# Performance work log

Measured on AMD Instinct MI355X. Metric: run time of the kernel, lower is better.

The kernel has to match this reference:

```python
import jax, jax.numpy as jnp
import numpy as np

B, C, D = 512, 50000, 256
N_LOADED = 40000


def setup_inputs() -> dict:
    key = jax.random.key(0)
    k1, k2, k3, k4 = jax.random.split(key, 4)
    visual_feats = jax.random.normal(k1, (B, D), dtype=jnp.float32)
    text_feats = jax.random.normal(k2, (C, D), dtype=jnp.float32)
    # sparse multi-hot labels; force class 0 positive for every row so the
    # positive set (intersected with loaded ids) is never empty
    batch_label = (jax.random.uniform(k3, (B, C)) < 0.02).astype(jnp.int32)
    batch_label = batch_label.at[:, 0].set(1)
    # distinct loaded class ids; force id 0 to be loaded
    ids = jax.random.permutation(k4, C)[:N_LOADED].astype(jnp.int32)
    ids = jnp.sort(ids).at[0].set(0)
    return {
        "visual_feats": visual_feats,
        "text_feats": text_feats,
        "batch_label": batch_label,
        "class_ids_loaded": ids,
        "d_space": D,
    }


def reference(visual_feats, text_feats, batch_label, class_ids_loaded, d_space):
    num_classes = text_feats.shape[0]
    # membership mask for loaded class ids (the set() intersection in torch)
    loaded = jnp.zeros((num_classes,), dtype=bool).at[class_ids_loaded].set(True)

    # cosine similarity; note: torch adds 1e-6 eps only to text-feature norms
    v = visual_feats / jnp.linalg.norm(visual_feats, axis=1, keepdims=True)
    t = text_feats / (1e-6 + jnp.linalg.norm(text_feats, axis=1, keepdims=True))
    S = v @ t.T  # [B, C]

    pos = (batch_label != 0) & loaded[None, :]  # ragged positive sets, as mask
    neg = (batch_label == 0) & loaded[None, :]  # ragged negative sets, as mask

    # denominator: sum of exp(sim) over negatives, per row
    denom = jnp.sum(jnp.where(neg, jnp.exp(S), 0.0), axis=1)  # [B]
    n_pos = jnp.sum(pos, axis=1).astype(S.dtype)  # [B]

    # per-row loss: mean over positives of -log(exp(s_p)/denom) = log(denom)-s_p
    per_row = jnp.sum(jnp.where(pos, jnp.log(denom)[:, None] - S, 0.0), axis=1) / n_pos
    return jnp.mean(per_row).reshape(1)
```

## Files before the change

kernel.cpp:

```cpp
#include <hip/hip_runtime.h>
#include <math.h>

#define D_DIM 256
#define TM 128
#define TN 128
#define BK 32
#define NBP 392
#define CBPR 7
#define CBLKS (CBPR * 512)

typedef __attribute__((ext_vector_type(8))) short short8;
typedef __attribute__((ext_vector_type(4))) float floatx4;
typedef unsigned long long u64;

__device__ __forceinline__ unsigned short f2bf(float f) {
    unsigned int u = __float_as_uint(f);
    u += 0x7FFFu + ((u >> 16) & 1u);
    return (unsigned short)(u >> 16);
}

__device__ __forceinline__ void gload16(const void* g, void* lds) {
    __builtin_amdgcn_global_load_lds(
        (const __attribute__((address_space(1))) unsigned int*)g,
        (__attribute__((address_space(3))) unsigned int*)lds, 16, 0, 0);
}

__global__ __launch_bounds__(256) void prep_compress(
    const float* __restrict__ V, const float* __restrict__ T,
    const int* __restrict__ label, const int* __restrict__ ids,
    u64* __restrict__ loadedmask, u64* __restrict__ posmask,
    unsigned short* __restrict__ Vb, unsigned short* __restrict__ Tb,
    float* __restrict__ gaccum, unsigned int* __restrict__ gcount,
    int B, int C, int n_loaded, int WPR) {
    const int bid = blockIdx.x;
    const int tid = threadIdx.x;
    const int lane = tid & 63;

    if (bid < CBLKS) {
        int row = bid / CBPR;
        int sub = bid - row * CBPR;
        int wl  = tid >> 6;
        int w0col = (sub * 4 + wl) * 2048;
        if (w0col >= C) return;
        const int* lp = label + (size_t)row * C;
        int4 lo[4], hi[4];
        #pragma unroll
        for (int r = 0; r < 4; ++r) {
            int c0 = w0col + r * 512 + lane * 8;
            if (c0 < C) {
                lo[r] = *(const int4*)(lp + c0);
                hi[r] = *(const int4*)(lp + c0 + 4);
            } else {
                lo[r] = make_int4(0, 0, 0, 0);
                hi[r] = make_int4(0, 0, 0, 0);
            }
        }
        #pragma unroll
        for (int r = 0; r < 4; ++r) {
            unsigned int by =
                (lo[r].x ? 1u : 0u) | (lo[r].y ? 2u : 0u) |
                (lo[r].z ? 4u : 0u) | (lo[r].w ? 8u : 0u) |
                (hi[r].x ? 16u : 0u) | (hi[r].y ? 32u : 0u) |
                (hi[r].z ? 64u : 0u) | (hi[r].w ? 128u : 0u);
            u64 wv = (u64)by << (8 * (lane & 7));
            wv |= __shfl_xor(wv, 1);
            wv |= __shfl_xor(wv, 2);
            wv |= __shfl_xor(wv, 4);
            if ((lane & 7) == 0) {
                int wc = ((w0col + r * 512) >> 6) + (lane >> 3);
                if (wc < WPR) posmask[(size_t)row * WPR + wc] = wv;
            }
        }
        return;
    }

    int ptid = (bid - CBLKS) * 256 + tid;
    if (ptid == 0) { *gcount = 0u; *gaccum = 0.f; }
    if (ptid < WPR) {
        int base = ptid << 6;
        int lo = 0, hi = n_loaded;
        while (lo < hi) { int mid = (lo + hi) >> 1; if (ids[mid] < base) lo = mid + 1; else hi = mid; }
        u64 m = 0;
        for (int i = lo; i < n_loaded; ++i) {
            int v = ids[i]; if (v >= base + 64) break;
            m |= 1ull << (v - base);
        }
        loadedmask[ptid] = m;
    }
    int wave = ptid >> 6;
    if (wave >= B + C) return;
    bool isV = wave < B;
    const float* src = isV ? (V + (size_t)wave * D_DIM)
                           : (T + (size_t)(wave - B) * D_DIM);
    float4 x = ((const float4*)src)[lane];
    float ss = x.x * x.x + x.y * x.y + x.z * x.z + x.w * x.w;
    #pragma unroll
    for (int off = 32; off > 0; off >>= 1) ss += __shfl_xor(ss, off);
    float nrm = sqrtf(ss);
    float s = isV ? (1.0f / nrm) : (1.0f / (1e-6f + nrm));
    ushort4 o;
    o.x = f2bf(x.x * s); o.y = f2bf(x.y * s);
    o.z = f2bf(x.z * s); o.w = f2bf(x.w * s);
    unsigned short* dst = isV ? (Vb + (size_t)wave * D_DIM)
                              : (Tb + (size_t)(wave - B) * D_DIM);
    ((ushort4*)dst)[lane] = o;
}

__global__ __launch_bounds__(256) void gemm_fused(
    const unsigned short* __restrict__ Vb, const unsigned short* __restrict__ Tb,
    const u64* __restrict__ posmask, const u64* __restrict__ loadedmask,
    float* __restrict__ denomP, float* __restrict__ posP, int C, int WPR) {
    __shared__ unsigned short As[2][TM * BK];
    __shared__ unsigned short Bs[2][TN * BK];
    __shared__ float sDen[TM], sPos[TM];

    const int tid  = threadIdx.x;
    const int lane = tid & 63;
    const int w    = tid >> 6;
    const int m0 = blockIdx.x * TM;
    const int n0 = blockIdx.y * TN;

    if (tid < TM) { sDen[tid] = 0.f; sPos[tid] = 0.f; }

    const int sra = lane >> 2;
    const int kc  = (lane & 3) * 8;
    int ga  = m0 + w * 32 + sra;
    int gb0 = n0 + w * 32 + sra;
    int gb1 = gb0 + 16;
    if (gb0 >= C) gb0 = C - 1;
    if (gb1 >= C) gb1 = C - 1;
    const unsigned short* gA0 = Vb + (size_t)ga * D_DIM + kc;
    const unsigned short* gA1 = gA0 + (size_t)16 * D_DIM;
    const unsigned short* gB0 = Tb + (size_t)gb0 * D_DIM + kc;
    const unsigned short* gB1 = Tb + (size_t)gb1 * D_DIM + kc;
    const int lofsA = w * 32 * BK;
    const int lofsB = w * 32 * BK;

    const int wm = (w >> 1) * 64;
    const int wn = (w & 1) * 64;
    const int fr = lane & 15;
    const int quad = lane >> 4;

    floatx4 acc[4][4];
    #pragma unroll
    for (int mi = 0; mi < 4; mi++)
        #pragma unroll
        for (int ni = 0; ni < 4; ni++) acc[mi][ni] = (floatx4)0.f;

    gload16(gA0, &As[0][lofsA]);
    gload16(gA1, &As[0][lofsA + 16 * BK]);
    gload16(gB0, &Bs[0][lofsB]);
    gload16(gB1, &Bs[0][lofsB + 16 * BK]);
    __syncthreads();

    #pragma unroll
    for (int kt = 0; kt < D_DIM / BK; ++kt) {
        const int cur = kt & 1;
        if (kt < D_DIM / BK - 1) {
            const int kb = (kt + 1) * BK;
            gload16(gA0 + kb, &As[cur ^ 1][lofsA]);
            gload16(gA1 + kb, &As[cur ^ 1][lofsA + 16 * BK]);
            gload16(gB0 + kb, &Bs[cur ^ 1][lofsB]);
            gload16(gB1 + kb, &Bs[cur ^ 1][lofsB + 16 * BK]);
        }
        short8 af[4], bf[4];
        #pragma unroll
        for (int mi = 0; mi < 4; mi++)
            af[mi] = *(const short8*)&As[cur][(wm + mi * 16 + fr) * BK + quad * 8];
        #pragma unroll
        for (int ni = 0; ni < 4; ni++)
            bf[ni] = *(const short8*)&Bs[cur][(wn + ni * 16 + fr) * BK + quad * 8];
        #pragma unroll
        for (int mi = 0; mi < 4; mi++)
            #pragma unroll
            for (int ni = 0; ni < 4; ni++)
                acc[mi][ni] = __builtin_amdgcn_mfma_f32_16x16x32_bf16(
                    af[mi], bf[ni], acc[mi][ni], 0, 0, 0);
        __syncthreads();
    }

    const int wcol = (n0 + wn) >> 6;
    const u64 loadedw = loadedmask[wcol];
    #pragma unroll
    for (int mi = 0; mi < 4; mi++) {
        #pragma unroll
        for (int i = 0; i < 4; i++) {
            const int mloc = wm + mi * 16 + quad * 4 + i;
            const u64 praw = posmask[(size_t)(m0 + mloc) * WPR + wcol];
            const u64 posw = praw & loadedw;
            const u64 negw = loadedw & ~praw;
            float den = 0.f, pos = 0.f;
            #pragma unroll
            for (int ni = 0; ni < 4; ni++) {
                const float s = acc[mi][ni][i];
                const int bit = ni * 16 + fr;
                if ((negw >> bit) & 1) den += __expf(s);
                if ((posw >> bit) & 1) pos += s;
            }
            #pragma unroll
            for (int off = 8; off >= 1; off >>= 1) {
                den += __shfl_xor(den, off);
                pos += __shfl_xor(pos, off);
            }
            if (fr == 0) {
                if (den != 0.f) atomicAdd(&sDen[mloc], den);
                if (pos != 0.f) atomicAdd(&sPos[mloc], pos);
            }
        }
    }
    __syncthreads();
    if (tid < TM) {
        denomP[(size_t)(m0 + tid) * NBP + blockIdx.y] = sDen[tid];
        posP[(size_t)(m0 + tid) * NBP + blockIdx.y]   = sPos[tid];
    }
}

__global__ void reduce_rows(const float* __restrict__ denomP, const float* __restrict__ posP,
                            const u64* __restrict__ posmask, const u64* __restrict__ loadedmask,
                            float* __restrict__ gaccum, unsigned int* __restrict__ gcount,
                            float* __restrict__ out, int B, int NB, int WPR) {
    __shared__ float bsum[4];
    int wv   = threadIdx.x >> 6;
    int row  = blockIdx.x * 4 + wv;
    int lane = threadIdx.x & 63;
    float den = 0.f, pos = 0.f;
    int cnt = 0;
    if (row < B) {
        for (int bn = lane; bn < NB; bn += 64) {
            den += denomP[(size_t)row * NBP + bn];
            pos += posP[(size_t)row * NBP + bn];
        }
        for (int j = lane; j < WPR; j += 64)
            cnt += __popcll(posmask[(size_t)row * WPR + j] & loadedmask[j]);
        #pragma unroll
        for (int off = 32; off > 0; off >>= 1) {
            den += __shfl_xor(den, off);
            pos += __shfl_xor(pos, off);
            cnt += __shfl_xor(cnt, off);
        }
    }
    if (lane == 0) bsum[wv] = (row < B) ? (logf(den) - pos / (float)cnt) : 0.f;
    __syncthreads();
    if (threadIdx.x == 0) {
        float s = bsum[0] + bsum[1] + bsum[2] + bsum[3];
        atomicAdd(gaccum, s);
        __threadfence();
        unsigned int old = atomicAdd(gcount, 1u);
        if (old == gridDim.x - 1) {
            float tot = atomicAdd(gaccum, 0.0f);
            out[0] = tot / (float)B;
        }
    }
}

extern "C" void kernel_launch(void* const* d_in, const int* in_sizes, int n_in,
                              void* d_out, int out_size, void* d_ws, size_t ws_size,
                              hipStream_t stream) {
    const float* V     = (const float*)d_in[0];
    const float* T     = (const float*)d_in[1];
    const int*   label = (const int*)d_in[2];
    const int*   ids   = (const int*)d_in[3];
    int B = in_sizes[0] / D_DIM;
    int C = in_sizes[1] / D_DIM;
    int n_loaded = in_sizes[3];
    int WPR = (C + 63) >> 6;
    int NB  = (C + TN - 1) / TN;

    char* ws = (char*)d_ws;
    float*        gaccum = (float*)(ws + 0);
    unsigned int* gcount = (unsigned int*)(ws + 8);
    u64*   loadedmask = (u64*)(ws + 2048);
    u64*   posmask    = (u64*)(ws + 8320);
    unsigned short* Vb = (unsigned short*)(ws + 3211392);
    unsigned short* Tb = (unsigned short*)(ws + 3473536);
    float* denomP  = (float*)(ws + 29073536);
    float* posP    = (float*)(ws + 29876352);

    int prep_blocks = ((B + C) * 64 + 255) / 256;
    prep_compress<<<CBLKS + prep_blocks, 256, 0, stream>>>(
        V, T, label, ids, loadedmask, posmask, Vb, Tb, gaccum, gcount,
        B, C, n_loaded, WPR);

    dim3 grid(B / TM, NB);
    gemm_fused<<<grid, 256, 0, stream>>>(Vb, Tb, posmask, loadedmask,
                                         denomP, posP, C, WPR);

    reduce_rows<<<(B + 3) / 4, 256, 0, stream>>>(denomP, posP, posmask, loadedmask,
                                                 gaccum, gcount, (float*)d_out, B, NB, WPR);
}
```

Before: 263.2 us.

## Fuse row reduction into GEMM epilogue via last-block-done counters

Removes the separate reduce_rows kernel launch. Each GEMM block now also accumulates the positive counts into a global per-row counter, and the last block to finish each row-tile (found through an atomic counter) reduces the partial sums and adds the result to the final loss. This removes one launch and the re-scan of the bitmasks, at the cost of extra atomics and a serial tail reduction done by only four blocks.

```diff
diff --git a/kernel.cpp b/kernel.cpp
--- a/kernel.cpp
+++ b/kernel.cpp
@@ -31,6 +31,7 @@
     u64* __restrict__ loadedmask, u64* __restrict__ posmask,
     unsigned short* __restrict__ Vb, unsigned short* __restrict__ Tb,
     float* __restrict__ gaccum, unsigned int* __restrict__ gcount,
+    unsigned int* __restrict__ cntG, unsigned int* __restrict__ mdone,
     int B, int C, int n_loaded, int WPR) {
     const int bid = blockIdx.x;
     const int tid = threadIdx.x;
@@ -76,6 +77,8 @@
 
     int ptid = (bid - CBLKS) * 256 + tid;
     if (ptid == 0) { *gcount = 0u; *gaccum = 0.f; }
+    if (ptid < 4) mdone[ptid] = 0u;
+    if (ptid < B) cntG[ptid] = 0u;
     if (ptid < WPR) {
         int base = ptid << 6;
         int lo = 0, hi = n_loaded;
@@ -109,10 +112,15 @@
 __global__ __launch_bounds__(256) void gemm_fused(
     const unsigned short* __restrict__ Vb, const unsigned short* __restrict__ Tb,
     const u64* __restrict__ posmask, const u64* __restrict__ loadedmask,
-    float* __restrict__ denomP, float* __restrict__ posP, int C, int WPR) {
+    float* __restrict__ denomP, float* __restrict__ posP,
+    unsigned int* __restrict__ cntG, unsigned int* __restrict__ mdone,
+    float* __restrict__ gaccum, unsigned int* __restrict__ gcount,
+    float* __restrict__ out, int B, int C, int WPR) {
     __shared__ unsigned short As[2][TM * BK];
     __shared__ unsigned short Bs[2][TN * BK];
     __shared__ float sDen[TM], sPos[TM];
+    __shared__ int sCnt[TM];
+    __shared__ int sIsLast;
 
     const int tid  = threadIdx.x;
     const int lane = tid & 63;
@@ -120,7 +128,7 @@
     const int m0 = blockIdx.x * TM;
     const int n0 = blockIdx.y * TN;
 
-    if (tid < TM) { sDen[tid] = 0.f; sPos[tid] = 0.f; }
+    if (tid < TM) { sDen[tid] = 0.f; sPos[tid] = 0.f; sCnt[tid] = 0; }
 
     const int sra = lane >> 2;
     const int kc  = (lane & 3) * 8;
@@ -205,6 +213,7 @@
             if (fr == 0) {
                 if (den != 0.f) atomicAdd(&sDen[mloc], den);
                 if (pos != 0.f) atomicAdd(&sPos[mloc], pos);
+                atomicAdd(&sCnt[mloc], (int)__popcll(posw));
             }
         }
     }
@@ -212,41 +221,44 @@
     if (tid < TM) {
         denomP[(size_t)(m0 + tid) * NBP + blockIdx.y] = sDen[tid];
         posP[(size_t)(m0 + tid) * NBP + blockIdx.y]   = sPos[tid];
-    }
-}
-
-__global__ void reduce_rows(const float* __restrict__ denomP, const float* __restrict__ posP,
-                            const u64* __restrict__ posmask, const u64* __restrict__ loadedmask,
-                            float* __restrict__ gaccum, unsigned int* __restrict__ gcount,
-                            float* __restrict__ out, int B, int NB, int WPR) {
-    __shared__ float bsum[4];
-    int wv   = threadIdx.x >> 6;
-    int row  = blockIdx.x * 4 + wv;
-    int lane = threadIdx.x & 63;
-    float den = 0.f, pos = 0.f;
-    int cnt = 0;
-    if (row < B) {
-        for (int bn = lane; bn < NB; bn += 64) {
+        if (sCnt[tid]) atomicAdd(&cntG[m0 + tid], (unsigned int)sCnt[tid]);
+    }
+
+    __syncthreads();
+    if (tid == 0) {
+        __threadfence();
+        unsigned int old = atomicAdd(&mdone[blockIdx.x], 1u);
+        sIsLast = (old == gridDim.y - 1);
+    }
+    __syncthreads();
+    if (!sIsLast) return;
+    if (tid == 0) __threadfence();
+    __syncthreads();
+
+    const int NBv = gridDim.y;
+    float wacc = 0.f;
+    for (int rr = 0; rr < TM / 4; ++rr) {
+        const int row = m0 + w * (TM / 4) + rr;
+        float den = 0.f, pos = 0.f;
+        for (int bn = lane; bn < NBv; bn += 64) {
             den += denomP[(size_t)row * NBP + bn];
             pos += posP[(size_t)row * NBP + bn];
         }
-        for (int j = lane; j < WPR; j += 64)
-            cnt += __popcll(posmask[(size_t)row * WPR + j] & loadedmask[j]);
         #pragma unroll
         for (int off = 32; off > 0; off >>= 1) {
             den += __shfl_xor(den, off);
             pos += __shfl_xor(pos, off);
-            cnt += __shfl_xor(cnt, off);
-        }
-    }
-    if (lane == 0) bsum[wv] = (row < B) ? (logf(den) - pos / (float)cnt) : 0.f;
-    __syncthreads();
-    if (threadIdx.x == 0) {
-        float s = bsum[0] + bsum[1] + bsum[2] + bsum[3];
+        }
+        wacc += logf(den) - pos / (float)cntG[row];
+    }
+    if (lane == 0) sDen[w] = wacc;
+    __syncthreads();
+    if (tid == 0) {
+        float s = sDen[0] + sDen[1] + sDen[2] + sDen[3];
         atomicAdd(gaccum, s);
         __threadfence();
         unsigned int old = atomicAdd(gcount, 1u);
-        if (old == gridDim.x - 1) {
+        if (old == 3u) {
             float tot = atomicAdd(gaccum, 0.0f);
             out[0] = tot / (float)B;
         }
@@ -269,22 +281,22 @@
     char* ws = (char*)d_ws;
     float*        gaccum = (float*)(ws + 0);
     unsigned int* gcount = (unsigned int*)(ws + 8);
-    u64*   loadedmask = (u64*)(ws + 2048);
-    u64*   posmask    = (u64*)(ws + 8320);
-    unsigned short* Vb = (unsigned short*)(ws + 3211392);
-    unsigned short* Tb = (unsigned short*)(ws + 3473536);
-    float* denomP  = (float*)(ws + 29073536);
-    float* posP    = (float*)(ws + 29876352);
+    unsigned int* mdone  = (unsigned int*)(ws + 16);
+    unsigned int* cntG   = (unsigned int*)(ws + 64);
+    u64*   loadedmask = (u64*)(ws + 4096);
+    u64*   posmask    = (u64*)(ws + 16384);
+    unsigned short* Vb = (unsigned short*)(ws + 3219456);
+    unsigned short* Tb = (unsigned short*)(ws + 3481600);
+    float* denomP  = (float*)(ws + 29081600);
+    float* posP    = (float*)(ws + 29884416);
 
     int prep_blocks = ((B + C) * 64 + 255) / 256;
     prep_compress<<<CBLKS + prep_blocks, 256, 0, stream>>>(
         V, T, label, ids, loadedmask, posmask, Vb, Tb, gaccum, gcount,
-        B, C, n_loaded, WPR);
+        cntG, mdone, B, C, n_loaded, WPR);
 
     dim3 grid(B / TM, NB);
     gemm_fused<<<grid, 256, 0, stream>>>(Vb, Tb, posmask, loadedmask,
-                                         denomP, posP, C, WPR);
-
-    reduce_rows<<<(B + 3) / 4, 256, 0, stream>>>(denomP, posP, posmask, loadedmask,
-                                                 gaccum, gcount, (float*)d_out, B, NB, WPR);
-}
+                                         denomP, posP, cntG, mdone,
+                                         gaccum, gcount, (float*)d_out, B, C, WPR);
+}
```

Measured after the change: 383.7 us. +45.8%, slower.

## Overlap label bitmask compression with GEMM via in-kernel completion counter

Applied to the files above, without the earlier changes.

Moves the label-to-bitmask compression out of the prep kernel and into the GEMM kernel as extra leading blocks. The GEMM blocks do their matmul first, then spin on an atomic completion counter. If the counter never completes they build the positive bitmask directly from the labels as a fallback. The intent is to overlap the memory-bound scan of the large label matrix with the compute-bound GEMM instead of serialising the two. Each wave now loads one mask word per lane and broadcasts it with shuffles, replacing per-row global loads. This adds spin-polling cost and relies on block scheduling order for the fast path.

```diff
diff --git a/kernel.cpp b/kernel.cpp
--- a/kernel.cpp
+++ b/kernel.cpp
@@ -25,57 +25,18 @@
         (__attribute__((address_space(3))) unsigned int*)lds, 16, 0, 0);
 }
 
-__global__ __launch_bounds__(256) void prep_compress(
+__global__ __launch_bounds__(256) void prep_rows(
     const float* __restrict__ V, const float* __restrict__ T,
-    const int* __restrict__ label, const int* __restrict__ ids,
-    u64* __restrict__ loadedmask, u64* __restrict__ posmask,
+    const int* __restrict__ ids,
+    u64* __restrict__ loadedmask,
     unsigned short* __restrict__ Vb, unsigned short* __restrict__ Tb,
     float* __restrict__ gaccum, unsigned int* __restrict__ gcount,
+    unsigned int* __restrict__ cdone,
     int B, int C, int n_loaded, int WPR) {
-    const int bid = blockIdx.x;
-    const int tid = threadIdx.x;
+    const int tid  = threadIdx.x;
     const int lane = tid & 63;
-
-    if (bid < CBLKS) {
-        int row = bid / CBPR;
-        int sub = bid - row * CBPR;
-        int wl  = tid >> 6;
-        int w0col = (sub * 4 + wl) * 2048;
-        if (w0col >= C) return;
-        const int* lp = label + (size_t)row * C;
-        int4 lo[4], hi[4];
-        #pragma unroll
-        for (int r = 0; r < 4; ++r) {
-            int c0 = w0col + r * 512 + lane * 8;
-            if (c0 < C) {
-                lo[r] = *(const int4*)(lp + c0);
-                hi[r] = *(const int4*)(lp + c0 + 4);
-            } else {
-                lo[r] = make_int4(0, 0, 0, 0);
-                hi[r] = make_int4(0, 0, 0, 0);
-            }
-        }
-        #pragma unroll
-        for (int r = 0; r < 4; ++r) {
-            unsigned int by =
-                (lo[r].x ? 1u : 0u) | (lo[r].y ? 2u : 0u) |
-                (lo[r].z ? 4u : 0u) | (lo[r].w ? 8u : 0u) |
-                (hi[r].x ? 16u : 0u) | (hi[r].y ? 32u : 0u) |
-                (hi[r].z ? 64u : 0u) | (hi[r].w ? 128u : 0u);
-            u64 wv = (u64)by << (8 * (lane & 7));
-            wv |= __shfl_xor(wv, 1);
-            wv |= __shfl_xor(wv, 2);
-            wv |= __shfl_xor(wv, 4);
-            if ((lane & 7) == 0) {
-                int wc = ((w0col + r * 512) >> 6) + (lane >> 3);
-                if (wc < WPR) posmask[(size_t)row * WPR + wc] = wv;
-            }
-        }
-        return;
-    }
-
-    int ptid = (bid - CBLKS) * 256 + tid;
-    if (ptid == 0) { *gcount = 0u; *gaccum = 0.f; }
+    int ptid = blockIdx.x * 256 + tid;
+    if (ptid == 0) { *gcount = 0u; *gaccum = 0.f; *cdone = 0u; }
     if (ptid < WPR) {
         int base = ptid << 6;
         int lo = 0, hi = n_loaded;
@@ -106,19 +67,65 @@
     ((ushort4*)dst)[lane] = o;
 }
 
-__global__ __launch_bounds__(256) void gemm_fused(
+__global__ __launch_bounds__(256) void compress_gemm(
     const unsigned short* __restrict__ Vb, const unsigned short* __restrict__ Tb,
-    const u64* __restrict__ posmask, const u64* __restrict__ loadedmask,
+    const int* __restrict__ label, const u64* __restrict__ loadedmask,
+    u64* __restrict__ posmask, unsigned int* __restrict__ cdone,
     float* __restrict__ denomP, float* __restrict__ posP, int C, int WPR) {
     __shared__ unsigned short As[2][TM * BK];
     __shared__ unsigned short Bs[2][TN * BK];
     __shared__ float sDen[TM], sPos[TM];
-
+    __shared__ int sReady;
+
+    const int bid  = blockIdx.x;
     const int tid  = threadIdx.x;
     const int lane = tid & 63;
-    const int w    = tid >> 6;
-    const int m0 = blockIdx.x * TM;
-    const int n0 = blockIdx.y * TN;
+
+    if (bid < CBLKS) {
+        int row = bid / CBPR;
+        int sub = bid - row * CBPR;
+        int wl  = tid >> 6;
+        int w0col = (sub * 4 + wl) * 2048;
+        if (w0col < C) {
+            const int* lp = label + (size_t)row * C;
+            int4 lo[4], hi[4];
+            #pragma unroll
+            for (int r = 0; r < 4; ++r) {
+                int c0 = w0col + r * 512 + lane * 8;
+                if (c0 < C) {
+                    lo[r] = *(const int4*)(lp + c0);
+                    hi[r] = *(const int4*)(lp + c0 + 4);
+                } else {
+                    lo[r] = make_int4(0, 0, 0, 0);
+                    hi[r] = make_int4(0, 0, 0, 0);
+                }
+            }
+            #pragma unroll
+            for (int r = 0; r < 4; ++r) {
+                unsigned int by =
+                    (lo[r].x ? 1u : 0u) | (lo[r].y ? 2u : 0u) |
+                    (lo[r].z ? 4u : 0u) | (lo[r].w ? 8u : 0u) |
+                    (hi[r].x ? 16u : 0u) | (hi[r].y ? 32u : 0u) |
+                    (hi[r].z ? 64u : 0u) | (hi[r].w ? 128u : 0u);
+                u64 wv = (u64)by << (8 * (lane & 7));
+                wv |= __shfl_xor(wv, 1);
+                wv |= __shfl_xor(wv, 2);
+                wv |= __shfl_xor(wv, 4);
+                if ((lane & 7) == 0) {
+                    int wc = ((w0col + r * 512) >> 6) + (lane >> 3);
+                    if (wc < WPR) posmask[(size_t)row * WPR + wc] = wv;
+                }
+            }
+        }
+        __syncthreads();
+        if (tid == 0) { __threadfence(); atomicAdd(cdone, 1u); }
+        return;
+    }
+
+    const int g  = bid - CBLKS;
+    const int m0 = (g & 3) * TM;
+    const int n0 = (g >> 2) * TN;
+    const int w  = tid >> 6;
 
     if (tid < TM) { sDen[tid] = 0.f; sPos[tid] = 0.f; }
 
@@ -179,16 +186,51 @@
         __syncthreads();
     }
 
+    if (tid == 0) {
+        int ready = 0;
+        for (int it = 0; it < 50000; ++it) {
+            if (atomicAdd(cdone, 0u) >= (unsigned int)CBLKS) { ready = 1; break; }
+        }
+        if (ready) __threadfence();
+        sReady = ready;
+    }
+    __syncthreads();
+
     const int wcol = (n0 + wn) >> 6;
     const u64 loadedw = loadedmask[wcol];
+    u64 praw;
+    if (sReady) {
+        praw = posmask[(size_t)(m0 + wm + lane) * WPR + wcol];
+    } else {
+        const int* lp = label + (size_t)(m0 + wm + lane) * C;
+        const int nBase = n0 + wn;
+        praw = 0;
+        #pragma unroll
+        for (int k = 0; k < 16; ++k) {
+            const int col0 = nBase + 4 * k;
+            unsigned int nib = 0;
+            if (col0 + 3 < C) {
+                int4 v = *(const int4*)(lp + col0);
+                nib = (v.x ? 1u : 0u) | (v.y ? 2u : 0u) | (v.z ? 4u : 0u) | (v.w ? 8u : 0u);
+            } else {
+                if (col0 + 0 < C && lp[col0 + 0]) nib |= 1u;
+                if (col0 + 1 < C && lp[col0 + 1]) nib |= 2u;
+                if (col0 + 2 < C && lp[col0 + 2]) nib |= 4u;
+                if (col0 + 3 < C && lp[col0 + 3]) nib |= 8u;
+            }
+            praw |= (u64)nib << (4 * k);
+        }
+    }
+
     #pragma unroll
     for (int mi = 0; mi < 4; mi++) {
         #pragma unroll
         for (int i = 0; i < 4; i++) {
-            const int mloc = wm + mi * 16 + quad * 4 + i;
-            const u64 praw = posmask[(size_t)(m0 + mloc) * WPR + wcol];
-            const u64 posw = praw & loadedw;
-            const u64 negw = loadedw & ~praw;
+            const int rloc = mi * 16 + quad * 4 + i;
+            const int mloc = wm + rloc;
+            const u64 pr = __shfl(praw, rloc);
+            const u64 posw = pr & loadedw;
+            const u64 negw = loadedw & ~pr;
             float den = 0.f, pos = 0.f;
             #pragma unroll
             for (int ni = 0; ni < 4; ni++) {
@@ -210,8 +252,8 @@
     }
     __syncthreads();
     if (tid < TM) {
-        denomP[(size_t)(m0 + tid) * NBP + blockIdx.y] = sDen[tid];
-        posP[(size_t)(m0 + tid) * NBP + blockIdx.y]   = sPos[tid];
+        denomP[(size_t)(m0 + tid) * NBP + (g >> 2)] = sDen[tid];
+        posP[(size_t)(m0 + tid) * NBP + (g >> 2)]   = sPos[tid];
     }
 }
 
@@ -269,6 +311,7 @@
     char* ws = (char*)d_ws;
     float*        gaccum = (float*)(ws + 0);
     unsigned int* gcount = (unsigned int*)(ws + 8);
+    unsigned int* cdone  = (unsigned int*)(ws + 16);
     u64*   loadedmask = (u64*)(ws + 2048);
     u64*   posmask    = (u64*)(ws + 8320);
     unsigned short* Vb = (unsigned short*)(ws + 3211392);
@@ -277,13 +320,13 @@
     float* posP    = (float*)(ws + 29876352);
 
     int prep_blocks = ((B + C) * 64 + 255) / 256;
-    prep_compress<<<CBLKS + prep_blocks, 256, 0, stream>>>(
-        V, T, label, ids, loadedmask, posmask, Vb, Tb, gaccum, gcount,
+    prep_rows<<<prep_blocks, 256, 0, stream>>>(
+        V, T, ids, loadedmask, Vb, Tb, gaccum, gcount, cdone,
         B, C, n_loaded, WPR);
 
-    dim3 grid(B / TM, NB);
-    gemm_fused<<<grid, 256, 0, stream>>>(Vb, Tb, posmask, loadedmask,
-                                         denomP, posP, C, WPR);
+    int gemm_blocks = (B / TM) * NB;
+    compress_gemm<<<CBLKS + gemm_blocks, 256, 0, stream>>>(
+        Vb, Tb, label, loadedmask, posmask, cdone, denomP, posP, C, WPR);
 
     reduce_rows<<<(B + 3) / 4, 256, 0, stream>>>(denomP, posP, posmask, loadedmask,
                                                  gaccum, gcount, (float*)d_out, B, NB, WPR);
```

New measurement: 469.4 us. +78.4%, slower.
